# Optimization experiments

Hardware: AMD Instinct MI355X
Metric: run time of the kernel (lower is better)

## Reference

```python
import jax, jax.numpy as jnp
import numpy as np

N_VARS = 16
BATCH = 16
SEQ = 512
P = N_VARS * (N_VARS - 1)  # ordered pairs i != j


def setup_inputs() -> dict:
    key = jax.random.key(0)
    ks = jax.random.split(key, 12)
    n = N_VARS

    def w(k, shape, fan_in):
        return jax.random.normal(k, shape, dtype=jnp.float32) / np.sqrt(fan_in)

    z = lambda *s: jnp.zeros(s, jnp.float32)
    return {
        'data': jax.random.normal(ks[0], (BATCH, SEQ, n), dtype=jnp.float32),
        # structure learner: n*n -> 256 -> 128 -> n*n (dropout skipped / eval mode)
        'Ws1': w(ks[1], (n * n, 256), n * n), 'bs1': z(256),
        'Ws2': w(ks[2], (256, 128), 256), 'bs2': z(128),
        'Ws3': w(ks[3], (128, n * n), 128), 'bs3': z(n * n),
        # per-variable causal mechanisms (stacked): (n-1) -> 128 -> 64 -> 1
        'Wm1': w(ks[4], (n, n - 1, 128), n - 1), 'bm1': z(n, 128),
        'Wm2': w(ks[5], (n, 128, 64), 128), 'bm2': z(n, 64),
        'Wm3': w(ks[6], (n, 64), 64), 'bm3': z(n),
        # per-pair independence tests (stacked): 2 -> 32 -> 1, sigmoid
        'Wt1': w(ks[7], (P, 2, 32), 2), 'bt1': z(P, 32),
        'Wt2': w(ks[8], (P, 32), 32), 'bt2': z(P),
    }


def reference(data, Ws1, bs1, Ws2, bs2, Ws3, bs3,
              Wm1, bm1, Wm2, bm2, Wm3, bm3,
              Wt1, bt1, Wt2, bt2):
    B, S, n = data.shape
    N = B * S
    flat = data.reshape(N, n)  # [N, n] all samples

    # ---- correlations of batch-averaged series (vectorized corrcoef) ----
    avg = data.mean(axis=0)                    # [S, n]
    xc = avg - avg.mean(axis=0, keepdims=True)
    cov = xc.T @ xc                            # [n, n]
    std = jnp.sqrt(jnp.clip(jnp.diag(cov), 0.0))
    denom = std[:, None] * std[None, :]
    corr = jnp.abs(jnp.where(denom > 0, cov / jnp.where(denom > 0, denom, 1.0), 0.0))
    corr = corr * (1.0 - jnp.eye(n, dtype=corr.dtype))  # zero diagonal (i != j only)

    # ---- structure learner MLP -> sigmoid -> strict upper-tri DAG mask ----
    h = jax.nn.relu(corr.reshape(1, -1) @ Ws1 + bs1)
    h = jax.nn.relu(h @ Ws2 + bs2)
    adj = jax.nn.sigmoid(h @ Ws3 + bs3).reshape(n, n)
    adj = jnp.triu(adj, 1)

    # ---- causal mechanisms: gather-parents -> per-var MLP -> scatter ----
    idx = np.stack([[j for j in range(n) if j != v] for v in range(n)])  # [n, n-1]
    pmask = adj > 0.5
    parent_mask = pmask[idx, np.arange(n)[:, None]].astype(flat.dtype)   # [n, n-1]
    inp = flat[:, idx] * parent_mask[None]                               # [N, n, n-1]
    h1 = jax.nn.relu(jnp.einsum('nvp,vph->nvh', inp, Wm1) + bm1)         # [N, n, 128]
    h2 = jax.nn.relu(jnp.einsum('nvh,vhk->nvk', h1, Wm2) + bm2)          # [N, n, 64]
    mech = jnp.einsum('nvk,vk->nv', h2, Wm3) + bm3                       # [N, n]
    has_parents = parent_mask.sum(axis=1) > 0                            # [n]
    predictions = jnp.where(has_parents[None, :], mech, flat).reshape(B, S, n)

    # ---- batched per-pair independence tests ----
    pairs = np.array([(i, j) for i in range(n) for j in range(n) if i != j])
    pi, pj = pairs[:, 0], pairs[:, 1]
    X = jnp.stack([flat[:, pi], flat[:, pj]], axis=-1)                   # [N, P, 2]
    ht = jax.nn.relu(jnp.einsum('npc,pch->nph', X, Wt1) + bt1)           # [N, P, 32]
    s = jax.nn.sigmoid(jnp.einsum('nph,ph->np', ht, Wt2) + bt2).mean(axis=0)  # [P]
    scores = jnp.zeros((n, n), flat.dtype).at[pi, pj].set(s)

    return adj, predictions, scores
```

## Files before the change

kernel.cpp:

```cpp
#include <hip/hip_runtime.h>
#include <hip/hip_bf16.h>


typedef __attribute__((ext_vector_type(8))) short bf16x8;
typedef __attribute__((ext_vector_type(4))) short bf16x4;
typedef __attribute__((ext_vector_type(4))) float f32x4;

#define DEV __device__ __forceinline__
DEV short f2bf(float f){ __hip_bfloat16 h = __float2bfloat16(f); short s; __builtin_memcpy(&s,&h,2); return s; }
DEV float bf2f(short s){ __hip_bfloat16 h; __builtin_memcpy(&h,&s,2); return __bfloat162float(h); }

struct GraphSm {
    float avT[16 * 532];
    float part[512];
    float cov[256];
    float corr[256];
    float h1[256];
    float h2[128];
    float adj[256];
    float m[16];
    float stdv[16];
};
struct MechSm {
    short W2T[64 * 136];
    short H1[4][16 * 136];
    float W1[16 * 128];
    float B1[128];
    float B2[64];
    float W3[64];
};
struct PairSm {
    float w0[32], w1[32], bb[32], w2[32];
    float red[256];
    float b2s;
};
union SmU { GraphSm g; MechSm m; PairSm p; };

__global__ void __launch_bounds__(256, 2) k_fused(
    const float* __restrict__ data,
    const float* __restrict__ Ws1, const float* __restrict__ bs1,
    const float* __restrict__ Ws2, const float* __restrict__ bs2,
    const float* __restrict__ Ws3, const float* __restrict__ bs3,
    const float* __restrict__ Wm1, const float* __restrict__ bm1,
    const float* __restrict__ Wm2, const float* __restrict__ bm2,
    const float* __restrict__ Wm3, const float* __restrict__ bm3,
    const float* __restrict__ Wt1, const float* __restrict__ bt1,
    const float* __restrict__ Wt2, const float* __restrict__ bt2,
    float* __restrict__ out)
{
    __shared__ __align__(16) SmU sm;
    __shared__ float pm_s[16];
    __shared__ float hp_s;
    int tid = threadIdx.x, bid = blockIdx.x;

    if (bid >= 256) {
        int p = bid - 256;
        int i = p / 15, jr = p % 15;
        int j = jr + (jr >= i ? 1 : 0);
        if (tid < 32) {
            sm.p.w0[tid] = Wt1[p*64 + tid];
            sm.p.w1[tid] = Wt1[p*64 + 32 + tid];
            sm.p.bb[tid] = bt1[p*32 + tid];
            sm.p.w2[tid] = Wt2[p*32 + tid];
        }
        if (tid == 0) sm.p.b2s = bt2[p];
        __syncthreads();
        float b2sv = sm.p.b2s;
        float acc = 0.f;
        for (int it = 0; it < 32; ++it) {
            int s = it*256 + tid;
            float xa = data[s*16 + i];
            float xb = data[s*16 + j];
            float z = b2sv;
            #pragma unroll
            for (int h = 0; h < 32; ++h) {
                float t1 = fmaf(xa, sm.p.w0[h], fmaf(xb, sm.p.w1[h], sm.p.bb[h]));
                z = fmaf(fmaxf(t1, 0.f), sm.p.w2[h], z);
            }
            acc += 1.f / (1.f + expf(-z));
        }
        sm.p.red[tid] = acc;
        __syncthreads();
        for (int off = 128; off > 0; off >>= 1) {
            if (tid < off) sm.p.red[tid] += sm.p.red[tid + off];
            __syncthreads();
        }
        if (tid == 0) out[256 + 131072 + i*16 + j] = sm.p.red[0] * (1.f/8192.f);
        return;
    }

    int v = bid >> 4, chunk = bid & 15;
    int gs0 = chunk * 512;

    {
        int vb = (tid & 3) * 4, sg = tid >> 2;
        for (int k = 0; k < 8; ++k) {
            int s = sg + k*64;
            float ax=0.f, ay=0.f, az=0.f, aw=0.f;
            #pragma unroll
            for (int b = 0; b < 16; ++b) {
                float4 d4 = *(const float4*)&data[b*8192 + s*16 + vb];
                ax += d4.x; ay += d4.y; az += d4.z; aw += d4.w;
            }
            sm.g.avT[(vb+0)*532 + s] = ax * 0.0625f;
            sm.g.avT[(vb+1)*532 + s] = ay * 0.0625f;
            sm.g.avT[(vb+2)*532 + s] = az * 0.0625f;
            sm.g.avT[(vb+3)*532 + s] = aw * 0.0625f;
        }
    }
    __syncthreads();
    if (tid < 128) {
        int vv = tid >> 3, sgm = tid & 7;
        const float* rp = &sm.g.avT[vv*532 + sgm*64];
        float a0=0.f, a1=0.f, a2=0.f, a3=0.f;
        for (int s = 0; s < 64; s += 4) {
            float4 fa = *(const float4*)&rp[s];
            a0 += fa.x; a1 += fa.y; a2 += fa.z; a3 += fa.w;
        }
        sm.g.part[tid] = (a0+a1)+(a2+a3);
    }
    __syncthreads();
    if (tid < 16) {
        float ms = 0.f;
        #pragma unroll
        for (int q = 0; q < 8; ++q) ms += sm.g.part[tid*8 + q];
        sm.g.m[tid] = ms * (1.f/512.f);
    }
    __syncthreads();
    {
        int ci = tid >> 4, cj = tid & 15;
        int slo = (ci <= cj) ? 0   : 256;
        int shi = (ci <  cj) ? 256 : 512;
        const float* pi_ = &sm.g.avT[ci*532];
        const float* pj_ = &sm.g.avT[cj*532];
        float a0=0.f, a1=0.f, a2=0.f, a3=0.f;
        for (int s = slo; s < shi; s += 4) {
            float4 fa = *(const float4*)&pi_[s];
            float4 fb = *(const float4*)&pj_[s];
            a0 = fmaf(fa.x, fb.x, a0); a1 = fmaf(fa.y, fb.y, a1);
            a2 = fmaf(fa.z, fb.z, a2); a3 = fmaf(fa.w, fb.w, a3);
        }
        sm.g.part[tid] = (a0+a1)+(a2+a3);
    }
    __syncthreads();
    {
        int ci = tid >> 4, cj = tid & 15;
        float raw = (ci == cj) ? sm.g.part[tid]
                               : sm.g.part[ci*16+cj] + sm.g.part[cj*16+ci];
        sm.g.cov[tid] = raw - 512.f * sm.g.m[ci] * sm.g.m[cj];
    }
    __syncthreads();
    if (tid < 16) sm.g.stdv[tid] = sqrtf(fmaxf(sm.g.cov[tid*17], 0.f));
    __syncthreads();
    {
        int ci = tid >> 4, cj = tid & 15;
        float den = sm.g.stdv[ci] * sm.g.stdv[cj];
        sm.g.corr[tid] = (den > 0.f && ci != cj) ? fabsf(sm.g.cov[tid]/den) : 0.f;
    }
    __syncthreads();
    {
        float a0=0.f, a1=0.f, a2=0.f, a3=0.f;
        const float* cp = sm.g.corr;
        #pragma unroll 4
        for (int k = 0; k < 256; k += 4) {
            a0 = fmaf(cp[k  ], Ws1[(k  )*256 + tid], a0);
            a1 = fmaf(cp[k+1], Ws1[(k+1)*256 + tid], a1);
            a2 = fmaf(cp[k+2], Ws1[(k+2)*256 + tid], a2);
            a3 = fmaf(cp[k+3], Ws1[(k+3)*256 + tid], a3);
        }
        sm.g.h1[tid] = fmaxf((a0+a1)+(a2+a3) + bs1[tid], 0.f);
    }
    __syncthreads();
    {
        int t = tid & 127, half = tid >> 7;
        const float* h1p = sm.g.h1 + half*128;
        const float* W2p = Ws2 + half*128*128;
        float a0=0.f, a1=0.f, a2=0.f, a3=0.f;
        #pragma unroll 4
        for (int k = 0; k < 128; k += 4) {
            a0 = fmaf(h1p[k  ], W2p[(k  )*128 + t], a0);
            a1 = fmaf(h1p[k+1], W2p[(k+1)*128 + t], a1);
            a2 = fmaf(h1p[k+2], W2p[(k+2)*128 + t], a2);
            a3 = fmaf(h1p[k+3], W2p[(k+3)*128 + t], a3);
        }
        sm.g.part[tid] = (a0+a1)+(a2+a3);
    }
    __syncthreads();
    if (tid < 128)
        sm.g.h2[tid] = fmaxf(sm.g.part[tid] + sm.g.part[128+tid] + bs2[tid], 0.f);
    __syncthreads();
    {
        float a0=0.f, a1=0.f, a2=0.f, a3=0.f;
        const float* h2p = sm.g.h2;
        #pragma unroll 4
        for (int k = 0; k < 128; k += 4) {
            a0 = fmaf(h2p[k  ], Ws3[(k  )*256 + tid], a0);
            a1 = fmaf(h2p[k+1], Ws3[(k+1)*256 + tid], a1);
            a2 = fmaf(h2p[k+2], Ws3[(k+2)*256 + tid], a2);
            a3 = fmaf(h2p[k+3], Ws3[(k+3)*256 + tid], a3);
        }
        float z = (a0+a1)+(a2+a3) + bs3[tid];
        float a = 1.f / (1.f + expf(-z));
        int r = tid >> 4, cc = tid & 15;
        float adjv = (r < cc) ? a : 0.f;
        sm.g.adj[tid] = adjv;
        if (bid == 0) out[tid] = adjv;
    }
    __syncthreads();
    if (tid < 15) {
        int jj = tid + (tid >= v ? 1 : 0);
        pm_s[tid] = (sm.g.adj[jj*16 + v] > 0.5f) ? 1.f : 0.f;
    }
    if (bid == 0 && tid >= 16 && tid < 32)
        out[256 + 131072 + (tid-16)*17] = 0.f;
    __syncthreads();
    if (tid == 0) {
        float s = 0.f;
        #pragma unroll
        for (int pr = 0; pr < 15; ++pr) s += pm_s[pr];
        hp_s = (s > 0.f) ? 1.f : 0.f;
    }
    __syncthreads();

    for (int e = tid; e < 2048; e += 256) {
        int k = e >> 7, h = e & 127;
        float val = 0.f;
        if (k != v) {
            int p = k - (k > v ? 1 : 0);
            val = Wm1[v*1920 + p*128 + h] * pm_s[p];
        }
        sm.m.W1[e] = val;
    }
    for (int e = tid; e < 8192; e += 256) {
        int h = e >> 6, jj2 = e & 63;
        sm.m.W2T[jj2*136 + h] = f2bf(Wm2[v*8192 + e]);
    }
    if (tid < 128) sm.m.B1[tid] = bm1[v*128 + tid];
    else if (tid < 192) sm.m.B2[tid - 128] = bm2[v*64 + tid - 128];
    else sm.m.W3[tid - 192] = Wm3[v*64 + tid - 192];
    __syncthreads();

    int lane = tid & 63, wid = tid >> 6;
    int c = lane & 15, q = lane >> 4;
    float hp = hp_s;
    float bm3v = bm3[v];

    bf16x8 a1f[8];
    #pragma unroll
    for (int ht = 0; ht < 8; ++ht) {
        #pragma unroll
        for (int jj = 0; jj < 8; ++jj) {
            int k = q*8 + jj;
            float w = (k < 16) ? sm.m.W1[k*128 + ht*16 + c] : 0.f;
            a1f[ht][jj] = f2bf(w);
        }
    }
    bf16x8 b2r[16];
    #pragma unroll
    for (int jt = 0; jt < 4; ++jt)
        #pragma unroll
        for (int ks = 0; ks < 4; ++ks)
            b2r[jt*4 + ks] = *(const bf16x8*)&sm.m.W2T[(jt*16 + c)*136 + ks*32 + q*8];
    float w3c[4], b2c[4];
    #pragma unroll
    for (int jt = 0; jt < 4; ++jt) { w3c[jt] = sm.m.W3[jt*16 + c]; b2c[jt] = sm.m.B2[jt*16 + c]; }

    short* h1buf = sm.m.H1[wid];

    for (int stl = 0; stl < 8; ++stl) {
        int st = wid*8 + stl;
        bf16x8 xb;
        #pragma unroll
        for (int i2 = 0; i2 < 8; ++i2) xb[i2] = 0;
        if (q < 2) {
            const float* xp = &data[(gs0 + st*16 + c)*16 + q*8];
            float4 u0 = *(const float4*)xp;
            float4 u1 = *(const float4*)(xp + 4);
            xb[0] = f2bf(u0.x); xb[1] = f2bf(u0.y);
            xb[2] = f2bf(u0.z); xb[3] = f2bf(u0.w);
            xb[4] = f2bf(u1.x); xb[5] = f2bf(u1.y);
            xb[6] = f2bf(u1.z); xb[7] = f2bf(u1.w);
        }
        f32x4 c1[8];
        #pragma unroll
        for (int ht = 0; ht < 8; ++ht) c1[ht] = *(const f32x4*)&sm.m.B1[ht*16 + q*4];
        #pragma unroll
        for (int ht = 0; ht < 8; ++ht)
            c1[ht] = __builtin_amdgcn_mfma_f32_16x16x32_bf16(a1f[ht], xb, c1[ht], 0, 0, 0);
        #pragma unroll
        for (int ht = 0; ht < 8; ++ht) {
            bf16x4 pk;
            #pragma unroll
            for (int r = 0; r < 4; ++r) pk[r] = f2bf(fmaxf(c1[ht][r], 0.f));
            *(bf16x4*)&h1buf[c*136 + ht*16 + q*4] = pk;
        }
        f32x4 c2[4];
        #pragma unroll
        for (int jt = 0; jt < 4; ++jt) {
            float bi = b2c[jt];
            c2[jt] = (f32x4){bi, bi, bi, bi};
        }
        #pragma unroll
        for (int ks = 0; ks < 4; ++ks) {
            bf16x8 a2 = *(const bf16x8*)&h1buf[c*136 + ks*32 + q*8];
            #pragma unroll
            for (int jt = 0; jt < 4; ++jt)
                c2[jt] = __builtin_amdgcn_mfma_f32_16x16x32_bf16(a2, b2r[jt*4 + ks], c2[jt], 0, 0, 0);
        }
        float part[4];
        #pragma unroll
        for (int r = 0; r < 4; ++r) part[r] = 0.f;
        #pragma unroll
        for (int jt = 0; jt < 4; ++jt)
            #pragma unroll
            for (int r = 0; r < 4; ++r)
                part[r] = fmaf(fmaxf(c2[jt][r], 0.f), w3c[jt], part[r]);
        #pragma unroll
        for (int off = 1; off < 16; off <<= 1)
            #pragma unroll
            for (int r = 0; r < 4; ++r)
                part[r] += __shfl_xor(part[r], off, 16);
        if (c == 0) {
            #pragma unroll
            for (int r = 0; r < 4; ++r) {
                int s_loc = st*16 + q*4 + r;
                float mech = part[r] + bm3v;
                float xv = data[(gs0 + s_loc)*16 + v];
                out[256 + (gs0 + s_loc)*16 + v] = (hp != 0.f) ? mech : xv;
            }
        }
    }
}

extern "C" void kernel_launch(void* const* d_in, const int* in_sizes, int n_in,
                              void* d_out, int out_size, void* d_ws, size_t ws_size,
                              hipStream_t stream)
{
    const float* data = (const float*)d_in[0];
    const float* Ws1  = (const float*)d_in[1];
    const float* bs1  = (const float*)d_in[2];
    const float* Ws2  = (const float*)d_in[3];
    const float* bs2  = (const float*)d_in[4];
    const float* Ws3  = (const float*)d_in[5];
    const float* bs3  = (const float*)d_in[6];
    const float* Wm1  = (const float*)d_in[7];
    const float* bm1  = (const float*)d_in[8];
    const float* Wm2  = (const float*)d_in[9];
    const float* bm2  = (const float*)d_in[10];
    const float* Wm3  = (const float*)d_in[11];
    const float* bm3  = (const float*)d_in[12];
    const float* Wt1  = (const float*)d_in[13];
    const float* bt1  = (const float*)d_in[14];
    const float* Wt2  = (const float*)d_in[15];
    const float* bt2  = (const float*)d_in[16];
    float* out = (float*)d_out;
    (void)d_ws; (void)ws_size;

    hipLaunchKernelGGL(k_fused, dim3(496), dim3(256), 0, stream,
                       data, Ws1, bs1, Ws2, bs2, Ws3, bs3,
                       Wm1, bm1, Wm2, bm2, Wm3, bm3,
                       Wt1, bt1, Wt2, bt2, out);
}
```

Measured before the change: 130.4 us.

## Double block size and quarter mechanism blocks to cut redundant graph recomputation

Mechanism blocks move from 16 sample chunks per variable to 4 larger chunks, with 512 threads per block. Every mechanism block recomputes the full correlation and structure MLP, so this removes three quarters of that redundant work. The structure MLP matmuls and covariance loop are split across the extra threads with partial-sum reductions. Pair-test blocks also go to 512 threads, use two independent accumulators and a fast exp with reciprocal. The cost is fewer blocks (304 against 496), which may leave compute units idle, and higher register pressure at 512 threads.

New measurement: 125.5 us. -3.8%, faster.

```diff
diff --git a/kernel.cpp b/kernel.cpp
--- a/kernel.cpp
+++ b/kernel.cpp
@@ -8,7 +8,6 @@
 
 #define DEV __device__ __forceinline__
 DEV short f2bf(float f){ __hip_bfloat16 h = __float2bfloat16(f); short s; __builtin_memcpy(&s,&h,2); return s; }
-DEV float bf2f(short s){ __hip_bfloat16 h; __builtin_memcpy(&h,&s,2); return __bfloat162float(h); }
 
 struct GraphSm {
     float avT[16 * 532];
@@ -23,7 +22,7 @@
 };
 struct MechSm {
     short W2T[64 * 136];
-    short H1[4][16 * 136];
+    short H1[8][16 * 136];
     float W1[16 * 128];
     float B1[128];
     float B2[64];
@@ -31,12 +30,12 @@
 };
 struct PairSm {
     float w0[32], w1[32], bb[32], w2[32];
-    float red[256];
+    float red[512];
     float b2s;
 };
 union SmU { GraphSm g; MechSm m; PairSm p; };
 
-__global__ void __launch_bounds__(256, 2) k_fused(
+__global__ void __launch_bounds__(512, 2) k_fused(
     const float* __restrict__ data,
     const float* __restrict__ Ws1, const float* __restrict__ bs1,
     const float* __restrict__ Ws2, const float* __restrict__ bs2,
@@ -53,8 +52,8 @@
     __shared__ float hp_s;
     int tid = threadIdx.x, bid = blockIdx.x;
 
-    if (bid >= 256) {
-        int p = bid - 256;
+    if (bid >= 64) {
+        int p = bid - 64;
         int i = p / 15, jr = p % 15;
         int j = jr + (jr >= i ? 1 : 0);
         if (tid < 32) {
@@ -67,21 +66,24 @@
         __syncthreads();
         float b2sv = sm.p.b2s;
         float acc = 0.f;
-        for (int it = 0; it < 32; ++it) {
-            int s = it*256 + tid;
+        for (int it = 0; it < 16; ++it) {
+            int s = it*512 + tid;
             float xa = data[s*16 + i];
             float xb = data[s*16 + j];
-            float z = b2sv;
-            #pragma unroll
-            for (int h = 0; h < 32; ++h) {
-                float t1 = fmaf(xa, sm.p.w0[h], fmaf(xb, sm.p.w1[h], sm.p.bb[h]));
-                z = fmaf(fmaxf(t1, 0.f), sm.p.w2[h], z);
+            float za = 0.f, zb = 0.f;
+            #pragma unroll
+            for (int h = 0; h < 32; h += 2) {
+                float t1 = fmaf(xa, sm.p.w0[h],   fmaf(xb, sm.p.w1[h],   sm.p.bb[h]));
+                za = fmaf(fmaxf(t1, 0.f), sm.p.w2[h],   za);
+                float t2 = fmaf(xa, sm.p.w0[h+1], fmaf(xb, sm.p.w1[h+1], sm.p.bb[h+1]));
+                zb = fmaf(fmaxf(t2, 0.f), sm.p.w2[h+1], zb);
             }
-            acc += 1.f / (1.f + expf(-z));
+            float z = b2sv + za + zb;
+            acc += __builtin_amdgcn_rcpf(1.f + __expf(-z));
         }
         sm.p.red[tid] = acc;
         __syncthreads();
-        for (int off = 128; off > 0; off >>= 1) {
+        for (int off = 256; off > 0; off >>= 1) {
             if (tid < off) sm.p.red[tid] += sm.p.red[tid + off];
             __syncthreads();
         }
@@ -89,13 +91,13 @@
         return;
     }
 
-    int v = bid >> 4, chunk = bid & 15;
-    int gs0 = chunk * 512;
+    int v = bid >> 2, chunk = bid & 3;
+    int gs0 = chunk * 2048;
 
     {
         int vb = (tid & 3) * 4, sg = tid >> 2;
-        for (int k = 0; k < 8; ++k) {
-            int s = sg + k*64;
+        for (int k = 0; k < 4; ++k) {
+            int s = sg + k*128;
             float ax=0.f, ay=0.f, az=0.f, aw=0.f;
             #pragma unroll
             for (int b = 0; b < 16; ++b) {
@@ -128,13 +130,12 @@
     }
     __syncthreads();
     {
-        int ci = tid >> 4, cj = tid & 15;
-        int slo = (ci <= cj) ? 0   : 256;
-        int shi = (ci <  cj) ? 256 : 512;
-        const float* pi_ = &sm.g.avT[ci*532];
-        const float* pj_ = &sm.g.avT[cj*532];
-        float a0=0.f, a1=0.f, a2=0.f, a3=0.f;
-        for (int s = slo; s < shi; s += 4) {
+        int t = tid & 255, hh = tid >> 8;
+        int ci = t >> 4, cj = t & 15;
+        const float* pi_ = &sm.g.avT[ci*532 + hh*256];
+        const float* pj_ = &sm.g.avT[cj*532 + hh*256];
+        float a0=0.f, a1=0.f, a2=0.f, a3=0.f;
+        for (int s = 0; s < 256; s += 4) {
             float4 fa = *(const float4*)&pi_[s];
             float4 fb = *(const float4*)&pj_[s];
             a0 = fmaf(fa.x, fb.x, a0); a1 = fmaf(fa.y, fb.y, a1);
@@ -143,63 +144,73 @@
         sm.g.part[tid] = (a0+a1)+(a2+a3);
     }
     __syncthreads();
-    {
+    if (tid < 256) {
         int ci = tid >> 4, cj = tid & 15;
-        float raw = (ci == cj) ? sm.g.part[tid]
-                               : sm.g.part[ci*16+cj] + sm.g.part[cj*16+ci];
-        sm.g.cov[tid] = raw - 512.f * sm.g.m[ci] * sm.g.m[cj];
+        sm.g.cov[tid] = sm.g.part[tid] + sm.g.part[256 + tid]
+                      - 512.f * sm.g.m[ci] * sm.g.m[cj];
     }
     __syncthreads();
     if (tid < 16) sm.g.stdv[tid] = sqrtf(fmaxf(sm.g.cov[tid*17], 0.f));
     __syncthreads();
-    {
+    if (tid < 256) {
         int ci = tid >> 4, cj = tid & 15;
         float den = sm.g.stdv[ci] * sm.g.stdv[cj];
         sm.g.corr[tid] = (den > 0.f && ci != cj) ? fabsf(sm.g.cov[tid]/den) : 0.f;
     }
     __syncthreads();
     {
-        float a0=0.f, a1=0.f, a2=0.f, a3=0.f;
-        const float* cp = sm.g.corr;
+        int t = tid & 255, half = tid >> 8;
+        const float* W1p = Ws1 + half*128*256;
+        const float* cp  = sm.g.corr + half*128;
+        float a0=0.f, a1=0.f, a2=0.f, a3=0.f;
+        #pragma unroll 8
+        for (int i = 0; i < 128; i += 4) {
+            a0 = fmaf(cp[i  ], W1p[(i  )*256 + t], a0);
+            a1 = fmaf(cp[i+1], W1p[(i+1)*256 + t], a1);
+            a2 = fmaf(cp[i+2], W1p[(i+2)*256 + t], a2);
+            a3 = fmaf(cp[i+3], W1p[(i+3)*256 + t], a3);
+        }
+        sm.g.part[half*256 + t] = (a0+a1)+(a2+a3);
+    }
+    __syncthreads();
+    if (tid < 256) sm.g.h1[tid] = fmaxf(sm.g.part[tid] + sm.g.part[256+tid] + bs1[tid], 0.f);
+    __syncthreads();
+    {
+        int t = tid & 127, qq = tid >> 7;
+        const float* W2p = Ws2 + qq*64*128;
+        const float* h1p = sm.g.h1 + qq*64;
+        float a0=0.f, a1=0.f, a2=0.f, a3=0.f;
         #pragma unroll 4
-        for (int k = 0; k < 256; k += 4) {
-            a0 = fmaf(cp[k  ], Ws1[(k  )*256 + tid], a0);
-            a1 = fmaf(cp[k+1], Ws1[(k+1)*256 + tid], a1);
-            a2 = fmaf(cp[k+2], Ws1[(k+2)*256 + tid], a2);
-            a3 = fmaf(cp[k+3], Ws1[(k+3)*256 + tid], a3);
-        }
-        sm.g.h1[tid] = fmaxf((a0+a1)+(a2+a3) + bs1[tid], 0.f);
-    }
-    __syncthreads();
-    {
-        int t = tid & 127, half = tid >> 7;
-        const float* h1p = sm.g.h1 + half*128;
-        const float* W2p = Ws2 + half*128*128;
+        for (int i = 0; i < 64; i += 4) {
+            a0 = fmaf(h1p[i  ], W2p[(i  )*128 + t], a0);
+            a1 = fmaf(h1p[i+1], W2p[(i+1)*128 + t], a1);
+            a2 = fmaf(h1p[i+2], W2p[(i+2)*128 + t], a2);
+            a3 = fmaf(h1p[i+3], W2p[(i+3)*128 + t], a3);
+        }
+        sm.g.part[qq*128 + t] = (a0+a1)+(a2+a3);
+    }
+    __syncthreads();
+    if (tid < 128)
+        sm.g.h2[tid] = fmaxf(sm.g.part[tid] + sm.g.part[128+tid] + sm.g.part[256+tid]
+                             + sm.g.part[384+tid] + bs2[tid], 0.f);
+    __syncthreads();
+    {
+        int t = tid & 255, half = tid >> 8;
+        const float* W3p = Ws3 + half*64*256;
+        const float* h2p = sm.g.h2 + half*64;
         float a0=0.f, a1=0.f, a2=0.f, a3=0.f;
         #pragma unroll 4
-        for (int k = 0; k < 128; k += 4) {
-            a0 = fmaf(h1p[k  ], W2p[(k  )*128 + t], a0);
-            a1 = fmaf(h1p[k+1], W2p[(k+1)*128 + t], a1);
-            a2 = fmaf(h1p[k+2], W2p[(k+2)*128 + t], a2);
-            a3 = fmaf(h1p[k+3], W2p[(k+3)*128 + t], a3);
-        }
-        sm.g.part[tid] = (a0+a1)+(a2+a3);
-    }
-    __syncthreads();
-    if (tid < 128)
-        sm.g.h2[tid] = fmaxf(sm.g.part[tid] + sm.g.part[128+tid] + bs2[tid], 0.f);
-    __syncthreads();
-    {
-        float a0=0.f, a1=0.f, a2=0.f, a3=0.f;
-        const float* h2p = sm.g.h2;
-        #pragma unroll 4
-        for (int k = 0; k < 128; k += 4) {
-            a0 = fmaf(h2p[k  ], Ws3[(k  )*256 + tid], a0);
-            a1 = fmaf(h2p[k+1], Ws3[(k+1)*256 + tid], a1);
-            a2 = fmaf(h2p[k+2], Ws3[(k+2)*256 + tid], a2);
-            a3 = fmaf(h2p[k+3], Ws3[(k+3)*256 + tid], a3);
-        }
-        float z = (a0+a1)+(a2+a3) + bs3[tid];
+        for (int i = 0; i < 64; i += 4) {
+            a0 = fmaf(h2p[i  ], W3p[(i  )*256 + t], a0);
+            a1 = fmaf(h2p[i+1], W3p[(i+1)*256 + t], a1);
+            a2 = fmaf(h2p[i+2], W3p[(i+2)*256 + t], a2);
+            a3 = fmaf(h2p[i+3], W3p[(i+3)*256 + t], a3);
+        }
+        sm.g.part[half*256 + t] = (a0+a1)+(a2+a3);
+    }
+    __syncthreads();
+    if (tid < 256) {
+        float z = sm.g.part[tid] + sm.g.part[256 + tid] + bs3[tid];
         float a = 1.f / (1.f + expf(-z));
         int r = tid >> 4, cc = tid & 15;
         float adjv = (r < cc) ? a : 0.f;
@@ -222,7 +233,7 @@
     }
     __syncthreads();
 
-    for (int e = tid; e < 2048; e += 256) {
+    for (int e = tid; e < 2048; e += 512) {
         int k = e >> 7, h = e & 127;
         float val = 0.f;
         if (k != v) {
@@ -231,13 +242,13 @@
         }
         sm.m.W1[e] = val;
     }
-    for (int e = tid; e < 8192; e += 256) {
+    for (int e = tid; e < 8192; e += 512) {
         int h = e >> 6, jj2 = e & 63;
         sm.m.W2T[jj2*136 + h] = f2bf(Wm2[v*8192 + e]);
     }
     if (tid < 128) sm.m.B1[tid] = bm1[v*128 + tid];
     else if (tid < 192) sm.m.B2[tid - 128] = bm2[v*64 + tid - 128];
-    else sm.m.W3[tid - 192] = Wm3[v*64 + tid - 192];
+    else if (tid < 256) sm.m.W3[tid - 192] = Wm3[v*64 + tid - 192];
     __syncthreads();
 
     int lane = tid & 63, wid = tid >> 6;
@@ -267,8 +278,8 @@
 
     short* h1buf = sm.m.H1[wid];
 
-    for (int stl = 0; stl < 8; ++stl) {
-        int st = wid*8 + stl;
+    for (int stl = 0; stl < 16; ++stl) {
+        int st = wid*16 + stl;
         bf16x8 xb;
         #pragma unroll
         for (int i2 = 0; i2 < 8; ++i2) xb[i2] = 0;
@@ -354,9 +365,9 @@
     const float* Wt2  = (const float*)d_in[15];
     const float* bt2  = (const float*)d_in[16];
     float* out = (float*)d_out;
-    (void)d_ws; (void)ws_size;
-
-    hipLaunchKernelGGL(k_fused, dim3(496), dim3(256), 0, stream,
+    (void)d_ws; (void)ws_size; (void)in_sizes; (void)n_in; (void)out_size;
+
+    hipLaunchKernelGGL(k_fused, dim3(304), dim3(512), 0, stream,
                        data, Ws1, bs1, Ws2, bs2, Ws3, bs3,
                        Wm1, bm1, Wm2, bm2, Wm3, bm3,
                        Wt1, bt1, Wt2, bt2, out);
```
